# Performance work log

Hardware: AMD Instinct MI355X
Metric: run time of the kernel (lower is better)

Reference implementation:

```python
import jax, jax.numpy as jnp
import numpy as np

K_SIZE = 7   # kernel_size
DIL = 2      # dilation
PAD = 6      # padding; satisfies 2*PAD == DIL*(K_SIZE-1) so unfold L == H*W


def _unfold(x, k, d, p):
    # Mimics F.pad(mode='replicate') + nn.Unfold(kernel, dilation=d, stride=1)
    # followed by view(B, C, k*k, H, W). Channel-major, kernel rows then cols.
    B, C, H, W = x.shape
    xp = jnp.pad(x, ((0, 0), (0, 0), (p, p), (p, p)), mode='edge')
    cols = jnp.stack(
        [xp[:, :, i * d:i * d + H, j * d:j * d + W]
         for i in range(k) for j in range(k)], axis=2)
    return cols  # [B, C, k*k, H, W]


def setup_inputs() -> dict:
    key = jax.random.key(0)
    ks = jax.random.split(key, 5)
    B, Cin, Cout, H, W = 2, 64, 64, 128, 128
    x = jax.random.normal(ks[0], (B, Cin, H, W), jnp.float32)
    s_in = 1.0 / np.sqrt(Cin)
    s_out = 1.0 / np.sqrt(Cout)
    Wk = jax.random.uniform(ks[1], (Cout, Cin), jnp.float32, -s_in, s_in)
    Wq = jax.random.uniform(ks[2], (Cout, Cin), jnp.float32, -s_in, s_in)
    Wv = jax.random.uniform(ks[3], (Cout, Cin), jnp.float32, -s_in, s_in)
    Wt = jax.random.uniform(ks[4], (Cin, Cout), jnp.float32, -s_out, s_out)
    return {"x": x, "Wk": Wk, "Wq": Wq, "Wv": Wv, "Wt": Wt}


def reference(x, Wk, Wq, Wv, Wt):
    # 1x1 convs (bias=False) as channel contractions + ReLU
    K = jax.nn.relu(jnp.einsum('oi,bihw->bohw', Wk, x))
    Q = jax.nn.relu(jnp.einsum('oi,bihw->bohw', Wq, x))
    V = jax.nn.relu(jnp.einsum('oi,bihw->bohw', Wv, x))
    Ku = _unfold(K, K_SIZE, DIL, PAD)   # [B, C, k2, H, W]
    Vu = _unfold(V, K_SIZE, DIL, PAD)   # [B, C, k2, H, W]
    # scores over the k2 dilated neighbors of each pixel (q dim == 1)
    A = jnp.einsum('bckhw,bchw->bkhw', Ku, Q)
    A = jax.nn.softmax(A, axis=1)       # softmax over k2 (torch dim=1)
    out = jnp.einsum('bckhw,bkhw->bchw', Vu, A)
    return jnp.einsum('oi,bihw->bohw', Wt, out) + x
```

## Files before the change

kernel.cpp:

```cpp
#include <hip/hip_runtime.h>
#include <hip/hip_bf16.h>

#define HH 128
#define WW 128
#define HWSZ (HH * WW)
#define CC 64
#define BB 2
#define KK 7
#define K2 49
#define ROWE 280

typedef unsigned int u32;

__device__ __forceinline__ int clampi(int v, int lo, int hi) {
    return v < lo ? lo : (v > hi ? hi : v);
}

__device__ __forceinline__ uint4 ld16(const __hip_bfloat16* src) {
    uint4 d; __builtin_memcpy(&d, src, 16); return d;
}

__device__ __forceinline__ void unpack8(uint4 d, float* f) {
    f[0] = __uint_as_float(d.x << 16); f[1] = __uint_as_float(d.x & 0xffff0000u);
    f[2] = __uint_as_float(d.y << 16); f[3] = __uint_as_float(d.y & 0xffff0000u);
    f[4] = __uint_as_float(d.z << 16); f[5] = __uint_as_float(d.z & 0xffff0000u);
    f[6] = __uint_as_float(d.w << 16); f[7] = __uint_as_float(d.w & 0xffff0000u);
}

__device__ __forceinline__ unsigned short f2bf(float v) {
    __hip_bfloat16 b = __float2bfloat16(v);
    return *reinterpret_cast<unsigned short*>(&b);
}

__device__ __forceinline__ int lane_off(int w) {
    const int parity = w & 1, t = w >> 1, phase = t & 1;
    return parity * 140 + phase * 70 + (t - phase);
}

__global__ __launch_bounds__(256) void kqv_kernel(
    const float* __restrict__ x,  const float* __restrict__ Wk,
    const float* __restrict__ Wq, const float* __restrict__ Wv,
    __hip_bfloat16* __restrict__ Kp, __hip_bfloat16* __restrict__ Qt,
    __hip_bfloat16* __restrict__ Vp)
{
    __shared__ __align__(16) float Wl[64][32];
    __shared__ __hip_bfloat16 T[32][2][128];

    const int xcd   = blockIdx.x & 7;
    const int t     = blockIdx.x >> 3;
    const int pbl   = t & 15;
    const int slice = t >> 4;
    const int pb    = xcd * 16 + pbl;
    const int a     = slice >> 1;
    const int ohb   = (slice & 1) * 32;
    const int b0    = pb >> 6;
    const int h0    = 2 * (pb & 63);
    const int hw0   = (pb & 63) * 256;

    const float* Wsel = (a == 0) ? Wk : (a == 1) ? Wq : Wv;

    for (int idx = threadIdx.x; idx < 2048; idx += 256) {
        const int c  = idx >> 5;
        const int ol = idx & 31;
        Wl[c][ol] = Wsel[(ohb + ol) * CC + c];
    }
    __syncthreads();

    const int quad = threadIdx.x & 63;
    const int oct  = threadIdx.x >> 6;

    const float* xbase = x + (size_t)b0 * CC * HWSZ + hw0 + quad * 4;

    float acc[8][4];
#pragma unroll
    for (int i = 0; i < 8; ++i)
#pragma unroll
        for (int j = 0; j < 4; ++j) acc[i][j] = 0.f;

#pragma unroll 4
    for (int c = 0; c < CC; ++c) {
        const float4 x4 = *(const float4*)(xbase + (size_t)c * HWSZ);
        const float xj[4] = {x4.x, x4.y, x4.z, x4.w};
        float w8[8];
        *(float4*)(w8)     = *(const float4*)&Wl[c][oct * 8];
        *(float4*)(w8 + 4) = *(const float4*)&Wl[c][oct * 8 + 4];
#pragma unroll
        for (int i = 0; i < 8; ++i)
#pragma unroll
            for (int j = 0; j < 4; ++j)
                acc[i][j] = fmaf(w8[i], xj[j], acc[i][j]);
    }

#pragma unroll
    for (int i = 0; i < 8; ++i) {
        const int ol = oct * 8 + i;
#pragma unroll
        for (int j = 0; j < 4; ++j) {
            const int px = quad * 4 + j;
            T[ol][px >> 7][px & 127] = __float2bfloat16(fmaxf(acc[i][j], 0.f));
        }
    }
    __syncthreads();

    if (a == 1) {
        for (int idx = threadIdx.x; idx < 1024; idx += 256) {
            const int px = idx >> 2;
            const int ck = idx & 3;
            unsigned short e[8];
#pragma unroll
            for (int u = 0; u < 8; ++u) {
                __hip_bfloat16 bv = T[ck * 8 + u][px >> 7][px & 127];
                e[u] = *reinterpret_cast<unsigned short*>(&bv);
            }
            __hip_bfloat16* dst = Qt +
                (size_t)(b0 * HWSZ + hw0 + px) * CC + ohb + ck * 8;
            __builtin_memcpy(dst, e, 16);
        }
    } else {
        __hip_bfloat16* arrp = (a == 0) ? Kp : Vp;
        for (int idx = threadIdx.x; idx < 2240; idx += 256) {
            const int row_id = idx / 35;
            const int cki    = idx - row_id * 35;
            const int ol     = row_id >> 1;
            const int rr     = row_id & 1;
            unsigned short e[8];
#pragma unroll
            for (int u = 0; u < 8; ++u) {
                const int q      = cki * 8 + u;
                const int parity = q >= 140 ? 1 : 0;
                const int sslot  = q - parity * 140;
                const int phase  = sslot >= 70 ? 1 : 0;
                const int local  = sslot - phase * 70;
                const int pix    = clampi(2 * (local - (phase ? 2 : 3)) + parity,
                                          0, 127);
                __hip_bfloat16 bv = T[ol][rr][pix];
                e[u] = *reinterpret_cast<unsigned short*>(&bv);
            }
            __hip_bfloat16* dst = arrp +
                ((size_t)(b0 * CC + ohb + ol) * HH + (h0 + rr)) * ROWE + cki * 8;
            __builtin_memcpy(dst, e, 16);
        }
    }
}

__global__ __launch_bounds__(256) void attn_kernel(
    const __hip_bfloat16* __restrict__ Kp, const __hip_bfloat16* __restrict__ Qt,
    const __hip_bfloat16* __restrict__ Vp, __hip_bfloat16* __restrict__ Ot)
{
    __shared__ float part[2][K2][33];

    const int xcd  = blockIdx.x & 7;
    const int s    = blockIdx.x >> 3;
    const int bh   = xcd * 32 + (s >> 2);
    const int wseg = s & 3;
    const int b    = bh >> 7;
    const int h    = bh & 127;

    const int tid = threadIdx.x;
    const int px  = (tid & 15) | ((tid >> 7) << 4);
    const int cq  = (tid >> 4) & 7;
    const int w   = wseg * 32 + px;
    const int p   = b * HWSZ + h * WW + w;
    const int c0  = cq * 8;

    int hn[KK];
#pragma unroll
    for (int i = 0; i < KK; ++i) hn[i] = clampi(h + 2 * i - 6, 0, HH - 1);

    const int loff = lane_off(w);
    const size_t cstride = (size_t)HH * ROWE;
    const __hip_bfloat16* Kc = Kp + (size_t)(b * CC + c0) * cstride + loff;
    const __hip_bfloat16* Vc = Vp + (size_t)(b * CC + c0) * cstride + loff;

    float qf[8];
    unpack8(ld16(Qt + (size_t)p * CC + c0), qf);

    float sc[K2];
#pragma unroll
    for (int k = 0; k < K2; ++k) sc[k] = 0.f;

    for (int ci = 0; ci < 8; ++ci) {
        uint4 kd[KK];
        const __hip_bfloat16* base = Kc + (size_t)ci * cstride;
#pragma unroll
        for (int i = 0; i < KK; ++i) kd[i] = ld16(base + (size_t)hn[i] * ROWE);
        const float qv = qf[ci];
#pragma unroll
        for (int i = 0; i < KK; ++i) {
            float kf[8];
            unpack8(kd[i], kf);
#pragma unroll
            for (int j = 0; j < KK; ++j)
                sc[i * KK + j] = fmaf(kf[j], qv, sc[i * KK + j]);
        }
    }

#pragma unroll
    for (int k = 0; k < K2; ++k) sc[k] += __shfl_xor(sc[k], 16, 64);
#pragma unroll
    for (int k = 0; k < K2; ++k) sc[k] += __shfl_xor(sc[k], 32, 64);

    const int sl = (tid >> 6) & 1;
    if (((tid >> 4) & 3) == 0) {
#pragma unroll
        for (int k = 0; k < K2; ++k) part[sl][k][px] = sc[k];
    }
    __syncthreads();

#pragma unroll
    for (int k = 0; k < K2; ++k) sc[k] = part[0][k][px] + part[1][k][px];
    float m = sc[0];
#pragma unroll
    for (int k = 1; k < K2; ++k) m = fmaxf(m, sc[k]);
    float sum = 0.f;
#pragma unroll
    for (int k = 0; k < K2; ++k) { sc[k] = __expf(sc[k] - m); sum += sc[k]; }
    const float inv = 1.f / sum;
#pragma unroll
    for (int k = 0; k < K2; ++k) sc[k] *= inv;

    unsigned short ob[8];
    for (int ci = 0; ci < 8; ++ci) {
        uint4 vd[KK];
        const __hip_bfloat16* base = Vc + (size_t)ci * cstride;
#pragma unroll
        for (int i = 0; i < KK; ++i) vd[i] = ld16(base + (size_t)hn[i] * ROWE);
        float acc = 0.f;
#pragma unroll
        for (int i = 0; i < KK; ++i) {
            float vf[8];
            unpack8(vd[i], vf);
#pragma unroll
            for (int j = 0; j < KK; ++j)
                acc = fmaf(vf[j], sc[i * KK + j], acc);
        }
        ob[ci] = f2bf(acc);
    }

    u32 od[4];
#pragma unroll
    for (int i = 0; i < 4; ++i)
        od[i] = (u32)ob[2 * i] | ((u32)ob[2 * i + 1] << 16);
    __builtin_memcpy(Ot + (size_t)p * CC + c0, od, 16);
}

__global__ __launch_bounds__(256) void wt_kernel(
    const __hip_bfloat16* __restrict__ Ot, const float* __restrict__ x,
    const float* __restrict__ Wt, float* __restrict__ out)
{
    const int xcd = blockIdx.x & 7;
    const int s   = blockIdx.x >> 3;
    const int pb  = xcd * 16 + (s & 15);
    const int og  = s >> 4;
    const int p   = pb * 256 + threadIdx.x;
    const int b   = p >> 14;
    const int hw  = p & 16383;
    const int o0  = og * 8;

    float fin[8];
#pragma unroll
    for (int i = 0; i < 8; ++i)
        fin[i] = x[((size_t)b * CC + o0 + i) * HWSZ + hw];

    const __hip_bfloat16* op = Ot + (size_t)p * CC;
#pragma unroll
    for (int k = 0; k < 8; ++k) {
        float oc[8];
        unpack8(ld16(op + 8 * k), oc);
#pragma unroll
        for (int cc = 0; cc < 8; ++cc) {
            const int c = 8 * k + cc;
#pragma unroll
            for (int i = 0; i < 8; ++i)
                fin[i] = fmaf(Wt[(o0 + i) * CC + c], oc[cc], fin[i]);
        }
    }

#pragma unroll
    for (int i = 0; i < 8; ++i)
        out[((size_t)b * CC + o0 + i) * HWSZ + hw] = fin[i];
}

extern "C" void kernel_launch(void* const* d_in, const int* in_sizes, int n_in,
                              void* d_out, int out_size, void* d_ws, size_t ws_size,
                              hipStream_t stream)
{
    const float* x  = (const float*)d_in[0];
    const float* Wk = (const float*)d_in[1];
    const float* Wq = (const float*)d_in[2];
    const float* Wv = (const float*)d_in[3];
    const float* Wt = (const float*)d_in[4];
    float* out = (float*)d_out;

    const size_t KP_ELEMS = (size_t)BB * CC * HH * ROWE;
    const size_t QT_ELEMS = (size_t)BB * HWSZ * CC;
    __hip_bfloat16* Kp = (__hip_bfloat16*)d_ws;
    __hip_bfloat16* Vp = Kp + KP_ELEMS;
    __hip_bfloat16* Qt = Vp + KP_ELEMS;
    __hip_bfloat16* Ot = Qt + QT_ELEMS;

    hipLaunchKernelGGL(kqv_kernel, dim3(768), dim3(256), 0, stream,
                       x, Wk, Wq, Wv, Kp, Qt, Vp);
    hipLaunchKernelGGL(attn_kernel, dim3(1024), dim3(256), 0, stream,
                       Kp, Qt, Vp, Ot);
    hipLaunchKernelGGL(wt_kernel, dim3(1024), dim3(256), 0, stream,
                       Ot, x, Wt, out);
}
```

Measured before the change: 72.01 us.

## Fuse output projection and residual into attention kernel via shared memory

Removes the separate wt_kernel launch and the bf16 Ot round trip through global memory. Each attention block stages its 32x64 output tile and the full 64x64 Wt matrix in LDS, then each thread computes 8 output channels plus the residual from x. This adds about 21KB of LDS per block and an extra Wt load in every block, which may lower occupancy of the attention kernel.

```diff
diff --git a/kernel.cpp b/kernel.cpp
--- a/kernel.cpp
+++ b/kernel.cpp
@@ -145,9 +145,12 @@
 
 __global__ __launch_bounds__(256) void attn_kernel(
     const __hip_bfloat16* __restrict__ Kp, const __hip_bfloat16* __restrict__ Qt,
-    const __hip_bfloat16* __restrict__ Vp, __hip_bfloat16* __restrict__ Ot)
+    const __hip_bfloat16* __restrict__ Vp, const float* __restrict__ Wt,
+    const float* __restrict__ x, float* __restrict__ out)
 {
     __shared__ float part[2][K2][33];
+    __shared__ __align__(16) float Wt_l[64][64];
+    __shared__ __align__(16) __hip_bfloat16 O_l[32][72];
 
     const int xcd  = blockIdx.x & 7;
     const int s    = blockIdx.x >> 3;
@@ -163,6 +166,9 @@
     const int p   = b * HWSZ + h * WW + w;
     const int c0  = cq * 8;
 
+    for (int idx = tid; idx < 4096; idx += 256)
+        Wt_l[idx >> 6][idx & 63] = Wt[idx];
+
     int hn[KK];
 #pragma unroll
     for (int i = 0; i < KK; ++i) hn[i] = clampi(h + 2 * i - 6, 0, HH - 1);
@@ -219,6 +225,12 @@
 #pragma unroll
     for (int k = 0; k < K2; ++k) sc[k] *= inv;
 
+    const int hw = h * WW + w;
+    float fin[8];
+#pragma unroll
+    for (int i = 0; i < 8; ++i)
+        fin[i] = x[((size_t)(b * CC) + c0 + i) * HWSZ + hw];
+
     unsigned short ob[8];
     for (int ci = 0; ci < 8; ++ci) {
         uint4 vd[KK];
@@ -241,44 +253,26 @@
 #pragma unroll
     for (int i = 0; i < 4; ++i)
         od[i] = (u32)ob[2 * i] | ((u32)ob[2 * i + 1] << 16);
-    __builtin_memcpy(Ot + (size_t)p * CC + c0, od, 16);
-}
-
-__global__ __launch_bounds__(256) void wt_kernel(
-    const __hip_bfloat16* __restrict__ Ot, const float* __restrict__ x,
-    const float* __restrict__ Wt, float* __restrict__ out)
-{
-    const int xcd = blockIdx.x & 7;
-    const int s   = blockIdx.x >> 3;
-    const int pb  = xcd * 16 + (s & 15);
-    const int og  = s >> 4;
-    const int p   = pb * 256 + threadIdx.x;
-    const int b   = p >> 14;
-    const int hw  = p & 16383;
-    const int o0  = og * 8;
-
-    float fin[8];
+    __builtin_memcpy(&O_l[px][c0], od, 16);
+    __syncthreads();
+
+#pragma unroll
+    for (int c8 = 0; c8 < 8; ++c8) {
+        uint4 d = *(const uint4*)&O_l[px][c8 * 8];
+        float oc[8];
+        unpack8(d, oc);
+#pragma unroll
+        for (int cc = 0; cc < 8; ++cc) {
+            const int c = c8 * 8 + cc;
+#pragma unroll
+            for (int i = 0; i < 8; ++i)
+                fin[i] = fmaf(Wt_l[c0 + i][c], oc[cc], fin[i]);
+        }
+    }
+
 #pragma unroll
     for (int i = 0; i < 8; ++i)
-        fin[i] = x[((size_t)b * CC + o0 + i) * HWSZ + hw];
-
-    const __hip_bfloat16* op = Ot + (size_t)p * CC;
-#pragma unroll
-    for (int k = 0; k < 8; ++k) {
-        float oc[8];
-        unpack8(ld16(op + 8 * k), oc);
-#pragma unroll
-        for (int cc = 0; cc < 8; ++cc) {
-            const int c = 8 * k + cc;
-#pragma unroll
-            for (int i = 0; i < 8; ++i)
-                fin[i] = fmaf(Wt[(o0 + i) * CC + c], oc[cc], fin[i]);
-        }
-    }
-
-#pragma unroll
-    for (int i = 0; i < 8; ++i)
-        out[((size_t)b * CC + o0 + i) * HWSZ + hw] = fin[i];
+        out[((size_t)(b * CC) + c0 + i) * HWSZ + hw] = fin[i];
 }
 
 extern "C" void kernel_launch(void* const* d_in, const int* in_sizes, int n_in,
@@ -293,16 +287,12 @@
     float* out = (float*)d_out;
 
     const size_t KP_ELEMS = (size_t)BB * CC * HH * ROWE;
-    const size_t QT_ELEMS = (size_t)BB * HWSZ * CC;
     __hip_bfloat16* Kp = (__hip_bfloat16*)d_ws;
     __hip_bfloat16* Vp = Kp + KP_ELEMS;
     __hip_bfloat16* Qt = Vp + KP_ELEMS;
-    __hip_bfloat16* Ot = Qt + QT_ELEMS;
 
     hipLaunchKernelGGL(kqv_kernel, dim3(768), dim3(256), 0, stream,
                        x, Wk, Wq, Wv, Kp, Qt, Vp);
     hipLaunchKernelGGL(attn_kernel, dim3(1024), dim3(256), 0, stream,
-                       Kp, Qt, Vp, Ot);
-    hipLaunchKernelGGL(wt_kernel, dim3(1024), dim3(256), 0, stream,
-                       Ot, x, Wt, out);
-}
+                       Kp, Qt, Vp, Wt, x, out);
+}
```

Result: faster. 64.85 us (-9.9%).
